# Performance work log

Measured on AMD Instinct MI355X. Metric: run time of the kernel, lower is better.

Reference implementation:

```python
import jax, jax.numpy as jnp
import numpy as np

B, S, H = 4, 2048, 2048
NH, NKV, HD = 16, 8, 128
Q_SIZE, KV_SIZE = NH * HD, NKV * HD
EPS = 1e-6
BASE = 10000.0
SCALE = HD ** -0.5


def _rmsnorm(x, w):
    # per-head RMSNorm over last dim (head_dim), with learnable weight
    var = jnp.mean(x * x, axis=-1, keepdims=True)
    return x * jax.lax.rsqrt(var + EPS) * w


def _rope(x, positions):
    # neox-style rotary embedding, rotary_dim == head_dim. x: [B,S,h,HD]
    half = HD // 2
    inv_freq = 1.0 / (BASE ** (jnp.arange(half, dtype=jnp.float32) / half))
    ang = positions.astype(jnp.float32)[..., None] * inv_freq  # [B,S,half]
    cos = jnp.cos(ang)[:, :, None, :]
    sin = jnp.sin(ang)[:, :, None, :]
    x1, x2 = x[..., :half], x[..., half:]
    return jnp.concatenate([x1 * cos - x2 * sin, x2 * cos + x1 * sin], axis=-1)


def setup_inputs() -> dict:
    key = jax.random.key(0)
    k0, k1, k2 = jax.random.split(key, 3)
    return {
        "positions": jnp.tile(jnp.arange(S, dtype=jnp.int32), (B, 1)),
        "hidden_states": jax.random.normal(k0, (B, S, H), jnp.float32),
        "w_qkv": jax.random.normal(k1, (H, Q_SIZE + 2 * KV_SIZE), jnp.float32) * (H ** -0.5),
        "q_norm_w": jnp.ones((HD,), jnp.float32),
        "k_norm_w": jnp.ones((HD,), jnp.float32),
        "w_o": jax.random.normal(k2, (NH * HD, H), jnp.float32) * ((NH * HD) ** -0.5),
    }


def reference(positions, hidden_states, w_qkv, q_norm_w, k_norm_w, w_o):
    # QKV projection (bias=False)
    qkv = jnp.einsum("bsh,ho->bso", hidden_states, w_qkv)
    q, k, v = jnp.split(qkv, [Q_SIZE, Q_SIZE + KV_SIZE], axis=-1)
    q = q.reshape(B, S, NH, HD)
    k = k.reshape(B, S, NKV, HD)
    v = v.reshape(B, S, NKV, HD)
    # qk-norm (RMSNorm per head vector)
    q = _rmsnorm(q, q_norm_w)
    k = _rmsnorm(k, k_norm_w)
    # rotary embeddings
    q = _rope(q, positions)
    k = _rope(k, positions)
    # GQA: repeat kv heads to match query heads
    rep = NH // NKV
    k = jnp.repeat(k, rep, axis=2)  # [B,S,NH,HD]
    v = jnp.repeat(v, rep, axis=2)
    # bidirectional (ENCODER_ONLY) attention, no mask
    scores = jnp.einsum("bqhd,bkhd->bhqk", q, k) * SCALE
    probs = jax.nn.softmax(scores, axis=-1)
    ctx = jnp.einsum("bhqk,bkhd->bqhd", probs, v).reshape(B, S, NH * HD)
    # output projection (bias=False)
    return jnp.einsum("bso,oh->bsh", ctx, w_o)
```

## Files before the change

### kernel.cpp

```cpp
#include <hip/hip_runtime.h>

#define S_LEN 2048
#define QKV_N 4096
#define SCALE_Q_LOG2E 0.12751744461f

typedef __attribute__((ext_vector_type(8))) short short8;
typedef __attribute__((ext_vector_type(4))) float f32x4;
typedef __attribute__((ext_vector_type(16))) float f32x16;
typedef __attribute__((ext_vector_type(4))) float floatv4;
typedef __attribute__((ext_vector_type(4))) unsigned short ushortv4;
typedef __attribute__((ext_vector_type(2))) unsigned int uint2v;

__device__ __forceinline__ float bf2f(unsigned short u) {
  union { unsigned u; float f; } x; x.u = ((unsigned)u) << 16; return x.f;
}
__device__ __forceinline__ unsigned short f2bf(float f) {
  union { float f; unsigned u; } x; x.f = f;
  unsigned r = x.u + 0x7fffu + ((x.u >> 16) & 1u);
  return (unsigned short)(r >> 16);
}

typedef const unsigned int __attribute__((address_space(1)))* gas1_t;
typedef unsigned int __attribute__((address_space(3)))* las3_t;
#define GLL16(g, l) __builtin_amdgcn_global_load_lds((gas1_t)(const void*)(g), (las3_t)(void*)(l), 16, 0, 0)

#define EXP2F(x) __builtin_amdgcn_exp2f(x)

__global__ __launch_bounds__(256) void k_prep(const float* __restrict__ hidden,
                                              unsigned short* __restrict__ hA,
                                              const float* __restrict__ w_qkv,
                                              unsigned short* __restrict__ wqkvT,
                                              const float* __restrict__ w_o,
                                              unsigned short* __restrict__ woT) {
  __shared__ float t[64][65];
  const int blk = blockIdx.x;
  if (blk < 16384) {
    int i = blk * 256 + threadIdx.x;
    floatv4 v = ((const floatv4*)hidden)[i];
    ushortv4 o;
    o[0] = f2bf(v[0]); o[1] = f2bf(v[1]); o[2] = f2bf(v[2]); o[3] = f2bf(v[3]);
    ((ushortv4*)hA)[i] = o;
    return;
  }
  const float* in;
  unsigned short* out;
  int bx, by, R, C;
  if (blk < 18432) {
    in = w_qkv; out = wqkvT; R = 2048; C = 4096;
    int bi = blk - 16384; bx = bi & 63; by = bi >> 6;
  } else {
    in = w_o; out = woT; R = 2048; C = 2048;
    int bi = blk - 18432; bx = bi & 31; by = bi >> 5;
  }
#pragma unroll
  for (int i = 0; i < 16; ++i) {
    int idx = threadIdx.x + i * 256;
    int r = idx >> 6, c = idx & 63;
    t[r][c] = in[(size_t)(by * 64 + r) * C + bx * 64 + c];
  }
  __syncthreads();
#pragma unroll
  for (int i = 0; i < 16; ++i) {
    int idx = threadIdx.x + i * 256;
    int r = idx >> 6, c = idx & 63;
    out[(size_t)(bx * 64 + r) * R + by * 64 + c] = f2bf(t[c][r]);
  }
}

template <int OUT_BF16>
__global__ __launch_bounds__(512, 2) void k_gemm256(const unsigned short* __restrict__ A,
                                                    const unsigned short* __restrict__ BT,
                                                    void* __restrict__ Cout,
                                                    int M, int N, int K) {
  const int tid = threadIdx.x;
  const int lane = tid & 63;
  const int wid = tid >> 6;
  const int wr = wid >> 2;
  const int wc = wid & 3;
  const int lr = lane & 15, lg = lane >> 4;

  const int gx = gridDim.x;
  const int nwg = gx * gridDim.y;
  const int lid = blockIdx.y * gx + blockIdx.x;
  const int qc = nwg >> 3;
  const int swz = (lid & 7) * qc + (lid >> 3);
  const int row0 = (swz / gx) * 256, col0 = (swz % gx) * 256;

  __shared__ __align__(16) unsigned short As[2][256 * 64];
  __shared__ __align__(16) unsigned short Bs[2][256 * 64];

  f32x4 acc[8][4];
#pragma unroll
  for (int m = 0; m < 8; ++m)
#pragma unroll
    for (int n = 0; n < 4; ++n) acc[m][n] = (f32x4){0.f, 0.f, 0.f, 0.f};

  const int r1 = tid >> 3, c1 = tid & 7;
  const int r2 = (tid + 512) >> 3, c2 = (tid + 512) & 7;
  const size_t so1 = (size_t)r1 * K + (size_t)((c1 ^ (r1 & 7)) * 8);
  const size_t so2 = (size_t)r2 * K + (size_t)((c2 ^ (r2 & 7)) * 8);
  const unsigned ld1 = (unsigned)tid * 16, ld2 = (unsigned)(tid + 512) * 16;

  const unsigned short* Abase = A + (size_t)row0 * K;
  const unsigned short* Bbase = BT + (size_t)col0 * K;

  auto stage = [&](int ph, int kt, int buf) {
    const size_t hb = (size_t)(ph >> 1) * 128 * K + (size_t)kt * 64;
    const unsigned short* src;
    unsigned short* dst;
    if (ph & 1) { src = Bbase + hb; dst = &Bs[buf][(ph >> 1) * 128 * 64]; }
    else        { src = Abase + hb; dst = &As[buf][(ph >> 1) * 128 * 64]; }
    GLL16(src + so1, (char*)dst + ld1);
    GLL16(src + so2, (char*)dst + ld2);
  };

#pragma unroll
  for (int ph = 0; ph < 4; ++ph) stage(ph, 0, 0);
  asm volatile("s_waitcnt vmcnt(0)" ::: "memory");
  __builtin_amdgcn_s_barrier();

  const int NT = K >> 6;
  for (int t = 0; t < NT; ++t) {
    const int cur = t & 1;
    const char* Ab = (const char*)&As[cur][0];
    const char* Bb = (const char*)&Bs[cur][0];
    short8 bf[4];
#pragma unroll
    for (int p = 0; p < 4; ++p) {
      const int ks = p >> 1, half = p & 1;
      short8 af[4];
#pragma unroll
      for (int m = 0; m < 4; ++m) {
        int rA = wr * 128 + (half * 4 + m) * 16 + lr;
        af[m] = *(const short8*)(Ab +
                ((rA * 128 + (ks * 4 + lg) * 16) ^ ((rA & 7) << 4)));
      }
      if (half == 0) {
#pragma unroll
        for (int n = 0; n < 4; ++n) {
          int rB = wc * 64 + n * 16 + lr;
          bf[n] = *(const short8*)(Bb +
                  ((rB * 128 + (ks * 4 + lg) * 16) ^ ((rB & 7) << 4)));
        }
      }
      if (t + 1 < NT) stage(p, t + 1, cur ^ 1);
      __builtin_amdgcn_sched_barrier(0);
      __builtin_amdgcn_s_setprio(1);
#pragma unroll
      for (int m = 0; m < 4; ++m)
#pragma unroll
        for (int n = 0; n < 4; ++n)
          acc[half * 4 + m][n] = __builtin_amdgcn_mfma_f32_16x16x32_bf16(
              af[m], bf[n], acc[half * 4 + m][n], 0, 0, 0);
      __builtin_amdgcn_s_setprio(0);
      if (p == 3) asm volatile("s_waitcnt vmcnt(0)" ::: "memory");
      __builtin_amdgcn_s_barrier();
    }
  }

  if (OUT_BF16) {
    unsigned short* C = (unsigned short*)Cout;
#pragma unroll
    for (int m = 0; m < 8; ++m)
#pragma unroll
      for (int n = 0; n < 4; ++n)
#pragma unroll
        for (int r = 0; r < 4; ++r)
          C[(size_t)(row0 + wr * 128 + m * 16 + 4 * lg + r) * N + col0 + wc * 64 + n * 16 + lr] =
              f2bf(acc[m][n][r]);
  } else {
    float* C = (float*)Cout;
#pragma unroll
    for (int m = 0; m < 8; ++m)
#pragma unroll
      for (int n = 0; n < 4; ++n)
#pragma unroll
        for (int r = 0; r < 4; ++r)
          C[(size_t)(row0 + wr * 128 + m * 16 + 4 * lg + r) * N + col0 + wc * 64 + n * 16 + lr] =
              acc[m][n][r];
  }
}

__global__ __launch_bounds__(256) void k_normrope(unsigned short* __restrict__ qkv,
                                                  const int* __restrict__ pos,
                                                  const float* __restrict__ qw,
                                                  const float* __restrict__ kw) {
  int lane = threadIdx.x & 63;
  int wv = (blockIdx.x << 2) + (threadIdx.x >> 6);
  int bs = wv / 24, hr = wv - bs * 24;
  bool isq = hr < 16;
  int col0 = isq ? hr * 128 : 2048 + (hr - 16) * 128;
  unsigned short* row = qkv + (size_t)bs * QKV_N + col0;
  float x1 = bf2f(row[lane]), x2 = bf2f(row[lane + 64]);
  float ss = x1 * x1 + x2 * x2;
#pragma unroll
  for (int m = 1; m < 64; m <<= 1) ss += __shfl_xor(ss, m, 64);
  float rn = rsqrtf(ss * (1.0f / 128.0f) + 1e-6f);
  const float* w = isq ? qw : kw;
  x1 *= rn * w[lane];
  x2 *= rn * w[lane + 64];
  float p = (float)pos[bs];
  float freq = exp2f(-(float)lane * 0.20762050593045951f);
  float ang = p * freq;
  float sn = __sinf(ang), cs = __cosf(ang);
  float o1 = x1 * cs - x2 * sn;
  float o2 = x2 * cs + x1 * sn;
  float sc = isq ? SCALE_Q_LOG2E : 1.0f;
  row[lane] = f2bf(o1 * sc);
  row[lane + 64] = f2bf(o2 * sc);
}

__global__ __launch_bounds__(512, 2) void k_attn(const unsigned short* __restrict__ qkv,
                                                 unsigned short* __restrict__ ctx) {
  const int tid = threadIdx.x;
  const int lane = tid & 63;
  const int wid = tid >> 6;
  const int hi = lane >> 5;
  const int l15 = lane & 15;
  const int q31 = lane & 31;
  const int lid0 = blockIdx.y * 8 + blockIdx.x;
  const int xcd = lid0 & 7, idx = lid0 >> 3;
  const int bh = xcd * 8 + (idx & 7);
  const int qb = idx >> 3;
  const int b = bh >> 4, h = bh & 15, kvh = h >> 1;

  __shared__ __align__(16) unsigned short Ks[2][64 * 128];
  __shared__ __align__(16) unsigned short Vs[2][64 * 128];

  const size_t baseRow = (size_t)b * S_LEN;
  const int qrow = qb * 256 + wid * 32 + q31;

  const unsigned short* Qg = qkv + (baseRow + qrow) * QKV_N + h * 128;
  short8 qf[8];
#pragma unroll
  for (int c = 0; c < 8; ++c)
    qf[c] = *(const short8*)(Qg + c * 16 + hi * 8);

  const unsigned short* Kg = qkv + baseRow * QKV_N + 2048 + kvh * 128;
  const unsigned short* Vg = Kg + 1024;

  size_t ksrc[2], vsrc[2];
  unsigned sdst[2];
#pragma unroll
  for (int i = 0; i < 2; ++i) {
    int s = tid + i * 512;
    int krow = s >> 4, kc = s & 15;
    ksrc[i] = (size_t)krow * QKV_N + (size_t)((kc ^ (krow & 7)) * 8);
    int st = s >> 3, in8 = s & 7;
    int vkey = (st >> 3) * 4 + (in8 >> 1);
    int vj = ((st & 7) << 1) | (in8 & 1);
    vsrc[i] = (size_t)vkey * QKV_N + (size_t)(vj * 8);
    sdst[i] = (unsigned)s * 16;
  }

#define STAGE(T, BUF)                                                    \
  {                                                                      \
    size_t toff = (size_t)(T) * 64 * QKV_N;                              \
    GLL16(Kg + toff + ksrc[0], (char*)Ks[BUF] + sdst[0]);                \
    GLL16(Kg + toff + ksrc[1], (char*)Ks[BUF] + sdst[1]);                \
    GLL16(Vg + toff + vsrc[0], (char*)Vs[BUF] + sdst[0]);                \
    GLL16(Vg + toff + vsrc[1], (char*)Vs[BUF] + sdst[1]);                \
  }

  f32x16 acc[4];
#pragma unroll
  for (int d = 0; d < 4; ++d)
#pragma unroll
    for (int r = 0; r < 16; ++r) acc[d][r] = 0.f;
  float m_run = -1e30f, l_run = 0.f;

  const unsigned vbase = (unsigned)(uintptr_t)&Vs[0][0];
  const int sw = (q31 & 7) << 4;

  auto tr_issue = [&](uint2v* vr, int ksg, unsigned vb) {
#pragma unroll
    for (int db = 0; db < 4; ++db)
#pragma unroll
      for (int rd = 0; rd < 2; ++rd) {
        int st = (ksg * 4 + hi * 2 + rd) * 8 + db * 2 + ((lane >> 4) & 1);
        unsigned a = vb + (unsigned)(st * 128 + l15 * 8);
        asm volatile("ds_read_b64_tr_b16 %0, %1" : "=v"(vr[db * 2 + rd]) : "v"(a));
      }
  };

  STAGE(0, 0);

  for (int t = 0; t < 32; ++t) {
    const int cur = t & 1;
    __builtin_amdgcn_s_barrier();
    __builtin_amdgcn_sched_barrier(0);
    if (t < 31) {
      STAGE(t + 1, cur ^ 1);
      asm volatile("s_waitcnt vmcnt(4)" ::: "memory");
    } else {
      asm volatile("s_waitcnt vmcnt(0)" ::: "memory");
    }
    __builtin_amdgcn_s_barrier();
    __builtin_amdgcn_sched_barrier(0);

    const char* Kb = (const char*)Ks[cur];
    f32x16 p0, p1;
#pragma unroll
    for (int r = 0; r < 16; ++r) { p0[r] = 0.f; p1[r] = 0.f; }
#pragma unroll
    for (int c = 0; c < 8; ++c) {
      int cb = c * 32 + hi * 16;
      short8 k0 = *(const short8*)(Kb + q31 * 256 + (cb ^ sw));
      short8 k1 = *(const short8*)(Kb + (32 + q31) * 256 + (cb ^ sw));
      p0 = __builtin_amdgcn_mfma_f32_32x32x16_bf16(k0, qf[c], p0, 0, 0, 0);
      p1 = __builtin_amdgcn_mfma_f32_32x32x16_bf16(k1, qf[c], p1, 0, 0, 0);
    }

    float mt = p0[0];
#pragma unroll
    for (int r = 1; r < 16; ++r) mt = fmaxf(mt, p0[r]);
#pragma unroll
    for (int r = 0; r < 16; ++r) mt = fmaxf(mt, p1[r]);
    mt = fmaxf(mt, __shfl_xor(mt, 32, 64));
    if (!__all(mt - m_run <= 8.0f)) {
      float mnew = fmaxf(m_run, mt);
      float corr = EXP2F(m_run - mnew);
      l_run *= corr;
#pragma unroll
      for (int d = 0; d < 4; ++d)
#pragma unroll
        for (int r = 0; r < 16; ++r) acc[d][r] *= corr;
      m_run = mnew;
    }
    float s_loc = 0.f;
#pragma unroll
    for (int r = 0; r < 16; ++r) { p0[r] = EXP2F(p0[r] - m_run); s_loc += p0[r]; }
#pragma unroll
    for (int r = 0; r < 16; ++r) { p1[r] = EXP2F(p1[r] - m_run); s_loc += p1[r]; }
    l_run += s_loc + __shfl_xor(s_loc, 32, 64);

    const unsigned vb = vbase + (unsigned)cur * 16384u;
    const float* pp0 = (const float*)&p0;
    const float* pp1 = (const float*)&p1;
    uint2v vrA[8], vrB[8];
    tr_issue(vrA, 0, vb);
#pragma unroll
    for (int ks = 0; ks < 4; ++ks) {
      const float* pr = ((ks & 2) ? pp1 : pp0) + (ks & 1) * 8;
      unsigned t0, t1, u0, u1;
      asm("v_cvt_pk_bf16_f32 %0, %1, %2" : "=v"(t0) : "v"(pr[0]), "v"(pr[1]));
      asm("v_cvt_pk_bf16_f32 %0, %1, %2" : "=v"(t1) : "v"(pr[2]), "v"(pr[3]));
      asm("v_cvt_pk_bf16_f32 %0, %1, %2" : "=v"(u0) : "v"(pr[4]), "v"(pr[5]));
      asm("v_cvt_pk_bf16_f32 %0, %1, %2" : "=v"(u1) : "v"(pr[6]), "v"(pr[7]));
      asm("v_permlane32_swap_b32 %0, %1" : "+v"(t0), "+v"(u0));
      asm("v_permlane32_swap_b32 %0, %1" : "+v"(t1), "+v"(u1));
      union { unsigned u[4]; short8 s; } pa;
      pa.u[0] = t0; pa.u[1] = t1; pa.u[2] = u0; pa.u[3] = u1;

      if (ks == 0) tr_issue(vrB, 1, vb);
      else if (ks == 1) tr_issue(vrA, 2, vb);
      else if (ks == 2) tr_issue(vrB, 3, vb);

      if (ks < 3) asm volatile("s_waitcnt lgkmcnt(8)" ::: "memory");
      else        asm volatile("s_waitcnt lgkmcnt(0)" ::: "memory");
      __builtin_amdgcn_sched_barrier(0);
#pragma unroll
      for (int db = 0; db < 4; ++db) {
        union { uint2v v[2]; short8 s; } vf;
        if (ks & 1) { vf.v[0] = vrB[db * 2]; vf.v[1] = vrB[db * 2 + 1]; }
        else        { vf.v[0] = vrA[db * 2]; vf.v[1] = vrA[db * 2 + 1]; }
        acc[db] = __builtin_amdgcn_mfma_f32_32x32x16_bf16(vf.s, pa.s, acc[db], 0, 0, 0);
      }
    }
  }

  float inv = 1.0f / l_run;
  unsigned short* Co = ctx + (baseRow + qrow) * 2048 + h * 128;
#pragma unroll
  for (int db = 0; db < 4; ++db)
#pragma unroll
    for (int g = 0; g < 4; ++g) {
      ushortv4 v;
#pragma unroll
      for (int j = 0; j < 4; ++j) v[j] = f2bf(acc[db][4 * g + j] * inv);
      *(ushortv4*)(Co + db * 32 + g * 8 + hi * 4) = v;
    }
#undef STAGE
}

extern "C" void kernel_launch(void* const* d_in, const int* in_sizes, int n_in,
                              void* d_out, int out_size, void* d_ws, size_t ws_size,
                              hipStream_t stream) {
  const int* positions = (const int*)d_in[0];
  const float* hidden = (const float*)d_in[1];
  const float* w_qkv = (const float*)d_in[2];
  const float* q_norm_w = (const float*)d_in[3];
  const float* k_norm_w = (const float*)d_in[4];
  const float* w_o = (const float*)d_in[5];
  float* out = (float*)d_out;

  char* ws = (char*)d_ws;
  unsigned short* hA    = (unsigned short*)(ws);
  unsigned short* wqkvT = (unsigned short*)(ws + 33554432);
  unsigned short* woT   = (unsigned short*)(ws + 50331648);
  unsigned short* qkv   = (unsigned short*)(ws + 58720256);
  unsigned short* ctx   = hA;

  k_prep<<<19456, 256, 0, stream>>>(hidden, hA, w_qkv, wqkvT, w_o, woT);
  k_gemm256<1><<<dim3(16, 32), 512, 0, stream>>>(hA, wqkvT, qkv, 8192, 4096, 2048);
  k_normrope<<<49152, 256, 0, stream>>>(qkv, positions, q_norm_w, k_norm_w);
  k_attn<<<dim3(8, 64), 512, 0, stream>>>(qkv, ctx);
  k_gemm256<0><<<dim3(8, 32), 512, 0, stream>>>(ctx, woT, out, 8192, 2048, 2048);
}
```

Before: 410.4 us.

## Fuse QK RMSNorm and RoPE into QKV GEMM epilogue with 4x2 wave layout

```diff
diff --git a/kernel.cpp b/kernel.cpp
--- a/kernel.cpp
+++ b/kernel.cpp
@@ -67,16 +67,19 @@
   }
 }
 
-template <int OUT_BF16>
+template <int MODE>
 __global__ __launch_bounds__(512, 2) void k_gemm256(const unsigned short* __restrict__ A,
                                                     const unsigned short* __restrict__ BT,
                                                     void* __restrict__ Cout,
-                                                    int M, int N, int K) {
+                                                    int M, int N, int K,
+                                                    const int* __restrict__ pos,
+                                                    const float* __restrict__ qw,
+                                                    const float* __restrict__ kw) {
   const int tid = threadIdx.x;
   const int lane = tid & 63;
   const int wid = tid >> 6;
-  const int wr = wid >> 2;
-  const int wc = wid & 3;
+  const int wr = wid >> 1;
+  const int wc = wid & 1;
   const int lr = lane & 15, lg = lane >> 4;
 
   const int gx = gridDim.x;
@@ -89,11 +92,11 @@
   __shared__ __align__(16) unsigned short As[2][256 * 64];
   __shared__ __align__(16) unsigned short Bs[2][256 * 64];
 
-  f32x4 acc[8][4];
-#pragma unroll
-  for (int m = 0; m < 8; ++m)
-#pragma unroll
-    for (int n = 0; n < 4; ++n) acc[m][n] = (f32x4){0.f, 0.f, 0.f, 0.f};
+  f32x4 acc[4][8];
+#pragma unroll
+  for (int m = 0; m < 4; ++m)
+#pragma unroll
+    for (int n = 0; n < 8; ++n) acc[m][n] = (f32x4){0.f, 0.f, 0.f, 0.f};
 
   const int r1 = tid >> 3, c1 = tid & 7;
   const int r2 = (tid + 512) >> 3, c2 = (tid + 512) & 7;
@@ -124,24 +127,24 @@
     const int cur = t & 1;
     const char* Ab = (const char*)&As[cur][0];
     const char* Bb = (const char*)&Bs[cur][0];
-    short8 bf[4];
+    short8 af[4];
 #pragma unroll
     for (int p = 0; p < 4; ++p) {
       const int ks = p >> 1, half = p & 1;
-      short8 af[4];
-#pragma unroll
-      for (int m = 0; m < 4; ++m) {
-        int rA = wr * 128 + (half * 4 + m) * 16 + lr;
-        af[m] = *(const short8*)(Ab +
-                ((rA * 128 + (ks * 4 + lg) * 16) ^ ((rA & 7) << 4)));
+      short8 bf[4];
+      if (half == 0) {
+#pragma unroll
+        for (int m = 0; m < 4; ++m) {
+          int rA = wr * 64 + m * 16 + lr;
+          af[m] = *(const short8*)(Ab +
+                  ((rA * 128 + (ks * 4 + lg) * 16) ^ ((rA & 7) << 4)));
+        }
       }
-      if (half == 0) {
-#pragma unroll
-        for (int n = 0; n < 4; ++n) {
-          int rB = wc * 64 + n * 16 + lr;
-          bf[n] = *(const short8*)(Bb +
-                  ((rB * 128 + (ks * 4 + lg) * 16) ^ ((rB & 7) << 4)));
-        }
+#pragma unroll
+      for (int n = 0; n < 4; ++n) {
+        int rB = wc * 128 + (half * 4 + n) * 16 + lr;
+        bf[n] = *(const short8*)(Bb +
+                ((rB * 128 + (ks * 4 + lg) * 16) ^ ((rB & 7) << 4)));
       }
       if (t + 1 < NT) stage(p, t + 1, cur ^ 1);
       __builtin_amdgcn_sched_barrier(0);
@@ -150,64 +153,71 @@
       for (int m = 0; m < 4; ++m)
 #pragma unroll
         for (int n = 0; n < 4; ++n)
-          acc[half * 4 + m][n] = __builtin_amdgcn_mfma_f32_16x16x32_bf16(
-              af[m], bf[n], acc[half * 4 + m][n], 0, 0, 0);
+          acc[m][half * 4 + n] = __builtin_amdgcn_mfma_f32_16x16x32_bf16(
+              af[m], bf[n], acc[m][half * 4 + n], 0, 0, 0);
       __builtin_amdgcn_s_setprio(0);
       if (p == 3) asm volatile("s_waitcnt vmcnt(0)" ::: "memory");
       __builtin_amdgcn_s_barrier();
     }
   }
 
-  if (OUT_BF16) {
+  if constexpr (MODE == 0) {
+    float* C = (float*)Cout;
+#pragma unroll
+    for (int m = 0; m < 4; ++m)
+#pragma unroll
+      for (int n = 0; n < 8; ++n)
+#pragma unroll
+        for (int r = 0; r < 4; ++r)
+          C[(size_t)(row0 + wr * 64 + m * 16 + 4 * lg + r) * N +
+            col0 + wc * 128 + n * 16 + lr] = acc[m][n][r];
+  } else {
     unsigned short* C = (unsigned short*)Cout;
-#pragma unroll
-    for (int m = 0; m < 8; ++m)
-#pragma unroll
-      for (int n = 0; n < 4; ++n)
-#pragma unroll
-        for (int r = 0; r < 4; ++r)
-          C[(size_t)(row0 + wr * 128 + m * 16 + 4 * lg + r) * N + col0 + wc * 64 + n * 16 + lr] =
-              f2bf(acc[m][n][r]);
-  } else {
-    float* C = (float*)Cout;
-#pragma unroll
-    for (int m = 0; m < 8; ++m)
-#pragma unroll
-      for (int n = 0; n < 4; ++n)
-#pragma unroll
-        for (int r = 0; r < 4; ++r)
-          C[(size_t)(row0 + wr * 128 + m * 16 + 4 * lg + r) * N + col0 + wc * 64 + n * 16 + lr] =
-              acc[m][n][r];
-  }
-}
-
-__global__ __launch_bounds__(256) void k_normrope(unsigned short* __restrict__ qkv,
-                                                  const int* __restrict__ pos,
-                                                  const float* __restrict__ qw,
-                                                  const float* __restrict__ kw) {
-  int lane = threadIdx.x & 63;
-  int wv = (blockIdx.x << 2) + (threadIdx.x >> 6);
-  int bs = wv / 24, hr = wv - bs * 24;
-  bool isq = hr < 16;
-  int col0 = isq ? hr * 128 : 2048 + (hr - 16) * 128;
-  unsigned short* row = qkv + (size_t)bs * QKV_N + col0;
-  float x1 = bf2f(row[lane]), x2 = bf2f(row[lane + 64]);
-  float ss = x1 * x1 + x2 * x2;
-#pragma unroll
-  for (int m = 1; m < 64; m <<= 1) ss += __shfl_xor(ss, m, 64);
-  float rn = rsqrtf(ss * (1.0f / 128.0f) + 1e-6f);
-  const float* w = isq ? qw : kw;
-  x1 *= rn * w[lane];
-  x2 *= rn * w[lane + 64];
-  float p = (float)pos[bs];
-  float freq = exp2f(-(float)lane * 0.20762050593045951f);
-  float ang = p * freq;
-  float sn = __sinf(ang), cs = __cosf(ang);
-  float o1 = x1 * cs - x2 * sn;
-  float o2 = x2 * cs + x1 * sn;
-  float sc = isq ? SCALE_Q_LOG2E : 1.0f;
-  row[lane] = f2bf(o1 * sc);
-  row[lane + 64] = f2bf(o2 * sc);
+    const int hcol0 = col0 + wc * 128;
+    if (col0 >= 3072) {
+#pragma unroll
+      for (int m = 0; m < 4; ++m)
+#pragma unroll
+        for (int n = 0; n < 8; ++n)
+#pragma unroll
+          for (int r = 0; r < 4; ++r)
+            C[(size_t)(row0 + wr * 64 + m * 16 + 4 * lg + r) * N +
+              hcol0 + n * 16 + lr] = f2bf(acc[m][n][r]);
+    } else {
+      const bool isq = (col0 < 2048);
+      const float scq = isq ? SCALE_Q_LOG2E : 1.0f;
+      const float* w = isq ? qw : kw;
+      float wv[8], fr[4];
+#pragma unroll
+      for (int n = 0; n < 8; ++n) wv[n] = w[n * 16 + lr];
+#pragma unroll
+      for (int j = 0; j < 4; ++j)
+        fr[j] = exp2f(-(float)(j * 16 + lr) * 0.20762050593045951f);
+#pragma unroll
+      for (int m = 0; m < 4; ++m)
+#pragma unroll
+        for (int r = 0; r < 4; ++r) {
+          const int row = row0 + wr * 64 + m * 16 + 4 * lg + r;
+          float ss = 0.f;
+#pragma unroll
+          for (int n = 0; n < 8; ++n) ss += acc[m][n][r] * acc[m][n][r];
+#pragma unroll
+          for (int st = 1; st < 16; st <<= 1) ss += __shfl_xor(ss, st, 64);
+          float rn = rsqrtf(ss * (1.0f / 128.0f) + 1e-6f);
+          float p = (float)pos[row];
+          unsigned short* Cr = C + (size_t)row * N + hcol0;
+#pragma unroll
+          for (int n = 0; n < 4; ++n) {
+            float x1 = acc[m][n][r] * rn * wv[n];
+            float x2 = acc[m][n + 4][r] * rn * wv[n + 4];
+            float ang = p * fr[n];
+            float cs = __cosf(ang), sn = __sinf(ang);
+            Cr[n * 16 + lr]       = f2bf((x1 * cs - x2 * sn) * scq);
+            Cr[(n + 4) * 16 + lr] = f2bf((x2 * cs + x1 * sn) * scq);
+          }
+        }
+    }
+  }
 }
 
 __global__ __launch_bounds__(512, 2) void k_attn(const unsigned short* __restrict__ qkv,
@@ -402,8 +412,9 @@
   unsigned short* ctx   = hA;
 
   k_prep<<<19456, 256, 0, stream>>>(hidden, hA, w_qkv, wqkvT, w_o, woT);
-  k_gemm256<1><<<dim3(16, 32), 512, 0, stream>>>(hA, wqkvT, qkv, 8192, 4096, 2048);
-  k_normrope<<<49152, 256, 0, stream>>>(qkv, positions, q_norm_w, k_norm_w);
+  k_gemm256<1><<<dim3(16, 32), 512, 0, stream>>>(hA, wqkvT, qkv, 8192, 4096, 2048,
+                                                 positions, q_norm_w, k_norm_w);
   k_attn<<<dim3(8, 64), 512, 0, stream>>>(qkv, ctx);
-  k_gemm256<0><<<dim3(8, 32), 512, 0, stream>>>(ctx, woT, out, 8192, 2048, 2048);
-}
+  k_gemm256<0><<<dim3(8, 32), 512, 0, stream>>>(ctx, woT, out, 8192, 2048, 2048,
+                                                nullptr, nullptr, nullptr);
+}
```

Result: faster. 379.4 us (-7.5%).
